# Performance work log

Measured on AMD Instinct MI355X. Metric: run time of the kernel, lower is better.

Reference implementation:

```python
import jax, jax.numpy as jnp
import numpy as np

EMBED_DIM = 1024
NUM_HEADS = 16
HEAD_DIM = EMBED_DIM // NUM_HEADS
BATCH = 2
SEQ = 2048


def setup_inputs() -> dict:
    key = jax.random.key(0)
    ks = jax.random.split(key, 10)
    s = 1.0 / np.sqrt(EMBED_DIM)
    inp = {
        "query": jax.random.normal(ks[0], (BATCH, SEQ, EMBED_DIM), jnp.float32),
        # Linear weights stored as [in, out] (y = x @ W + b)
        "wq": jax.random.normal(ks[1], (EMBED_DIM, EMBED_DIM), jnp.float32) * s,
        "bq": jnp.zeros((EMBED_DIM,), jnp.float32),
        "wk": jax.random.normal(ks[2], (EMBED_DIM, EMBED_DIM), jnp.float32) * s,
        "bk": jnp.zeros((EMBED_DIM,), jnp.float32),
        "wv": jax.random.normal(ks[3], (EMBED_DIM, EMBED_DIM), jnp.float32) * s,
        "bv": jnp.zeros((EMBED_DIM,), jnp.float32),
        "wo": jax.random.normal(ks[4], (EMBED_DIM, EMBED_DIM), jnp.float32) * s,
        "bo": jnp.zeros((EMBED_DIM,), jnp.float32),
        "temperature": jnp.float32(HEAD_DIM),  # learnable temperature, init = head_dim
    }
    return inp


def reference(query, wq, bq, wk, bk, wv, bv, wo, bo, temperature):
    B, S, E = query.shape
    # self-attention: key = value = query
    Q = (query @ wq + bq).reshape(B, S, NUM_HEADS, HEAD_DIM).transpose(0, 2, 1, 3)
    K = (query @ wk + bk).reshape(B, S, NUM_HEADS, HEAD_DIM).transpose(0, 2, 1, 3)
    V = (query @ wv + bv).reshape(B, S, NUM_HEADS, HEAD_DIM).transpose(0, 2, 1, 3)
    # squared Euclidean distances: ||q||^2 + ||k||^2 - 2<q,k>
    q_sq = jnp.sum(Q * Q, axis=-1, keepdims=True)          # (B,H,Sq,1)
    k_sq = jnp.sum(K * K, axis=-1, keepdims=True)          # (B,H,Sk,1)
    qk = jnp.einsum("bhqd,bhkd->bhqk", Q, K)
    d_sq = jnp.maximum(q_sq + jnp.swapaxes(k_sq, -2, -1) - 2.0 * qk, 0.0)
    attn = jax.nn.softmax(-d_sq / temperature, axis=-1)    # (B,H,Sq,Sk)
    out = jnp.einsum("bhqk,bhkd->bhqd", attn, V)
    out = out.transpose(0, 2, 1, 3).reshape(B, S, E)
    return out @ wo + bo
```

## Files before the change

kernel.cpp:

```cpp
#include <hip/hip_runtime.h>
#include <stdint.h>
#include <stddef.h>


#define LOG2E 1.44269504088896f

typedef __attribute__((ext_vector_type(8))) short bf16x8;
typedef __attribute__((ext_vector_type(4))) float f32x4;
typedef __attribute__((ext_vector_type(4))) unsigned short u16x4;

__device__ __forceinline__ unsigned short f2b(float f) {
  union { float f; unsigned int u; } x; x.f = f;
  unsigned int u = x.u;
  u += 0x7fffu + ((u >> 16) & 1u);
  return (unsigned short)(u >> 16);
}
__device__ __forceinline__ float b2f(unsigned short s) {
  union { unsigned int u; float f; } x; x.u = ((unsigned int)s) << 16;
  return x.f;
}
__device__ __forceinline__ unsigned int fbits(float f) {
  union { float f; unsigned int u; } x; x.f = f; return x.u;
}

#define GLD_LDS(g, l) __builtin_amdgcn_global_load_lds( \
    (const __attribute__((address_space(1))) void*)(g), \
    (__attribute__((address_space(3))) void*)(l), 16, 0, 0)

__global__ void prep_kernel(const float* __restrict__ X,
                            const float* __restrict__ wq, const float* __restrict__ wk,
                            const float* __restrict__ wv, const float* __restrict__ wo,
                            unsigned short* __restrict__ Xb,
                            unsigned short* __restrict__ WTqkv, unsigned short* __restrict__ WTo) {
  int z = blockIdx.z;
  if (z == 4) {
    size_t base = ((size_t)(blockIdx.y * 16 + blockIdx.x)) * 16384;
    #pragma unroll
    for (int j = 0; j < 16; ++j) {
      size_t i = base + (size_t)(j * 256 + threadIdx.x) * 4;
      f32x4 v = *(const f32x4*)&X[i];
      u16x4 o;
      #pragma unroll
      for (int k = 0; k < 4; ++k) o[k] = f2b(v[k]);
      *(u16x4*)&Xb[i] = o;
    }
    return;
  }
  __shared__ float tile[64][65];
  const float* src = (z == 0) ? wq : (z == 1) ? wk : (z == 2) ? wv : wo;
  unsigned short* dst = (z < 3) ? (WTqkv + (size_t)z * 1024 * 1024) : WTo;
  int k0 = blockIdx.y * 64, n0 = blockIdx.x * 64;
  int rr = threadIdx.x >> 6, cc = threadIdx.x & 63;
  #pragma unroll
  for (int p = 0; p < 16; ++p) {
    int row = p * 4 + rr;
    tile[row][cc] = src[(size_t)(k0 + row) * 1024 + n0 + cc];
  }
  __syncthreads();
  #pragma unroll
  for (int p = 0; p < 16; ++p) {
    int row = p * 4 + rr;
    dst[(size_t)(n0 + row) * 1024 + k0 + cc] = f2b(tile[cc][row]);
  }
}

__global__ __launch_bounds__(256, 3) void gemm_qkv_kernel(
    const unsigned short* __restrict__ X, const unsigned short* __restrict__ WT,
    const float* __restrict__ bq, const float* __restrict__ bk, const float* __restrict__ bv,
    const float* __restrict__ temp,
    unsigned short* __restrict__ Qb, unsigned short* __restrict__ Kb,
    unsigned short* __restrict__ VTo, float* __restrict__ ks2) {
  __shared__ __align__(16) unsigned short smem3[24576];
#define AS3(j) (smem3 + (j) * 4096)
#define BS3(j) (smem3 + 12288 + (j) * 4096)
  const int t = threadIdx.x, w = t >> 6, lane = t & 63;
  const int r = lane & 15, q4 = lane >> 4;
  const int m0 = blockIdx.y * 128, n0 = blockIdx.x * 128;
  const int wr = (w >> 1) * 64, wc = (w & 1) * 64;
  const unsigned short* Xg = X + (size_t)m0 * 1024;
  const unsigned short* Wg = WT + (size_t)n0 * 1024;
  const unsigned short* xs0 = Xg + (size_t)(t >> 2) * 1024 + (t & 3) * 8;
  const unsigned short* xs1 = xs0 + (size_t)64 * 1024;
  const unsigned short* ws0 = Wg + (size_t)(t >> 2) * 1024 + (t & 3) * 8;
  const unsigned short* ws1 = ws0 + (size_t)64 * 1024;
  f32x4 acc[4][4] = {};

#define QKV_STAGE(J2)                                     \
  {                                                       \
    GLD_LDS(xs0, &AS3(J2)[(w * 64) * 8]);                 \
    GLD_LDS(xs1, &AS3(J2)[(256 + w * 64) * 8]);           \
    GLD_LDS(ws0, &BS3(J2)[(w * 64) * 8]);                 \
    GLD_LDS(ws1, &BS3(J2)[(256 + w * 64) * 8]);           \
    xs0 += 32; xs1 += 32; ws0 += 32; ws1 += 32;           \
  }

  QKV_STAGE(0)
  QKV_STAGE(1)
  asm volatile("s_waitcnt vmcnt(4)" ::: "memory");
  __builtin_amdgcn_s_barrier();
  __builtin_amdgcn_sched_barrier(0);

#define QKV_BODY(J, STG, LAST)                                                \
  {                                                                           \
    if (STG) QKV_STAGE(((J) + 2) % 3)                                         \
    bf16x8 af[4], bfr[4];                                                     \
    _Pragma("unroll")                                                         \
    for (int mf = 0; mf < 4; ++mf)                                            \
      af[mf] = *(const bf16x8*)&AS3(J)[(wr + mf * 16 + r) * 32 + q4 * 8];     \
    _Pragma("unroll")                                                         \
    for (int nf = 0; nf < 4; ++nf)                                            \
      bfr[nf] = *(const bf16x8*)&BS3(J)[(wc + nf * 16 + r) * 32 + q4 * 8];    \
    _Pragma("unroll")                                                         \
    for (int mf = 0; mf < 4; ++mf)                                            \
      _Pragma("unroll")                                                       \
      for (int nf = 0; nf < 4; ++nf)                                          \
        acc[mf][nf] = __builtin_amdgcn_mfma_f32_16x16x32_bf16(af[mf], bfr[nf], acc[mf][nf], 0, 0, 0); \
    if (STG)       { asm volatile("s_waitcnt vmcnt(4)" ::: "memory"); }       \
    else if (!(LAST)) { asm volatile("s_waitcnt vmcnt(0)" ::: "memory"); }    \
    if (!(LAST)) {                                                            \
      __builtin_amdgcn_s_barrier();                                           \
      __builtin_amdgcn_sched_barrier(0);                                      \
    }                                                                         \
  }

  for (int hh = 0; hh < 5; ++hh) {
    QKV_BODY(0, 1, 0) QKV_BODY(1, 1, 0) QKV_BODY(2, 1, 0)
    QKV_BODY(0, 1, 0) QKV_BODY(1, 1, 0) QKV_BODY(2, 1, 0)
  }
  QKV_BODY(0, 0, 0)
  QKV_BODY(1, 0, 1)
  __syncthreads();
#undef QKV_BODY
#undef QKV_STAGE

  const int nblk = n0 >> 10;
  if (nblk == 0) {
    const int nc0 = n0 & 1023;
    #pragma unroll
    for (int nf = 0; nf < 4; ++nf) {
      int n = nc0 + wc + nf * 16 + r;
      float bb = bq[n];
      #pragma unroll
      for (int mf = 0; mf < 4; ++mf) {
        int m = m0 + wr + mf * 16 + q4 * 4;
        f32x4 v = acc[mf][nf];
        #pragma unroll
        for (int i = 0; i < 4; ++i)
          Qb[(size_t)(m + i) * 1024 + n] = f2b(v[i] + bb);
      }
    }
  } else if (nblk == 1) {
    const float sc = LOG2E / temp[0];
    const int nc0 = n0 & 1023;
    float s2a[4][4] = {};
    #pragma unroll
    for (int nf = 0; nf < 4; ++nf) {
      int n = nc0 + wc + nf * 16 + r;
      float bb = bk[n];
      #pragma unroll
      for (int mf = 0; mf < 4; ++mf) {
        int m = m0 + wr + mf * 16 + q4 * 4;
        f32x4 v = acc[mf][nf];
        #pragma unroll
        for (int i = 0; i < 4; ++i) {
          unsigned short os = f2b(v[i] + bb);
          Kb[(size_t)(m + i) * 1024 + n] = os;
          float xb = b2f(os);
          s2a[mf][i] += xb * xb;
        }
      }
    }
    #pragma unroll
    for (int mf = 0; mf < 4; ++mf)
      #pragma unroll
      for (int i = 0; i < 4; ++i) {
        float v = s2a[mf][i];
        v += __shfl_xor(v, 1, 64);
        v += __shfl_xor(v, 2, 64);
        v += __shfl_xor(v, 4, 64);
        v += __shfl_xor(v, 8, 64);
        s2a[mf][i] = v * sc;
      }
    if (r == 0) {
      int hh2 = (nc0 + wc) >> 6;
      #pragma unroll
      for (int mf = 0; mf < 4; ++mf) {
        int m = m0 + wr + mf * 16 + q4 * 4;
        int bb2 = m >> 11, ss = m & 2047;
        #pragma unroll
        for (int i = 0; i < 4; ++i)
          ks2[(size_t)(bb2 * 16 + hh2) * 2048 + ss + i] = s2a[mf][i];
      }
    }
  } else {
    unsigned short* Vt = smem3;
    const int c0 = n0 - 2048;
    const int head = w & 1;
    #pragma unroll
    for (int nf = 0; nf < 4; ++nf) {
      int c = c0 + wc + nf * 16 + r;
      float bb = bv[c];
      int d = c & 63;
      #pragma unroll
      for (int mf = 0; mf < 4; ++mf) {
        int mloc = wr + mf * 16 + q4 * 4;
        int G = mloc >> 6;
        int k6 = mloc & 63;
        int pos = (k6 >> 5) * 32 + ((k6 & 15) >> 2) * 8 + ((k6 >> 4) & 1) * 4;
        f32x4 v = acc[mf][nf];
        u16x4 pk;
        #pragma unroll
        for (int i = 0; i < 4; ++i) pk[i] = f2b(v[i] + bb);
        *(u16x4*)&Vt[(head * 64 + d) * 132 + G * 64 + pos] = pk;
      }
    }
    __syncthreads();
    int row = t >> 1, ch = t & 1;
    int hd = row >> 6, dd = row & 63;
    int hglob = (c0 >> 6) + hd;
    int bb2 = m0 >> 11, s0 = m0 & 2047;
    unsigned short* dst = &VTo[((size_t)((bb2 * 16 + hglob) * 64 + dd)) * 2048 + s0 + ch * 64];
    const unsigned short* srcL = &Vt[(hd * 64 + dd) * 132 + ch * 64];
    #pragma unroll
    for (int k2 = 0; k2 < 16; ++k2)
      *(u16x4*)&dst[k2 * 4] = *(const u16x4*)&srcL[k2 * 4];
  }
#undef AS3
#undef BS3
}

__global__ __launch_bounds__(256, 2) void flash_kernel(
    const unsigned short* __restrict__ Qb, const unsigned short* __restrict__ Kb,
    const unsigned short* __restrict__ VT, const float* __restrict__ ks2,
    const float* __restrict__ temp, unsigned short* __restrict__ AO) {
  __shared__ __align__(16) unsigned short Ks[2][64 * 64];
  __shared__ __align__(16) unsigned short Vs[3][64 * 64];
  __shared__ __align__(16) float KQs[2048];
  const int t = threadIdx.x, w = t >> 6, lane = t & 63;
  const int r = lane & 15, q4 = lane >> 4;
  const int wgid = blockIdx.x + 16 * blockIdx.y;
  const int xcd = wgid & 7, s = wgid >> 3;
  const int bh = xcd + 8 * (s & 3);
  const int b = bh >> 4, h = bh & 15;
  const int q0 = (s >> 2) * 128;
  const float cc = 2.0f * LOG2E / temp[0];

  bf16x8 qf[2][2];
  #pragma unroll
  for (int qg = 0; qg < 2; ++qg) {
    int sq = q0 + w * 32 + qg * 16 + r;
    const unsigned short* qp = Qb + (size_t)(b * 2048 + sq) * 1024 + h * 64;
    #pragma unroll
    for (int ks = 0; ks < 2; ++ks) qf[qg][ks] = *(const bf16x8*)(qp + ks * 32 + q4 * 8);
  }

  f32x4 accO[2][4] = {};
  f32x4 lsum[2] = {};
  bf16x8 ones;
  #pragma unroll
  for (int j = 0; j < 8; ++j) ones[j] = (short)0x3F80;

  const unsigned short* Kg = Kb + ((size_t)b * 2048) * 1024 + h * 64;
  const unsigned short* Vg = VT + ((size_t)bh * 64) * 2048;
  const float* kqb = ks2 + bh * 2048;

  const unsigned short* kp0 = Kg + (size_t)(t >> 2) * 1024 + (t & 3) * 8;
  const unsigned short* kp1 = kp0 + 32;
  int dd0 = t >> 3;
  const unsigned short* vp0 = Vg + (size_t)dd0 * 2048 + ((t & 7) ^ (dd0 & 7)) * 8;
  const unsigned short* vp1 = vp0 + (size_t)32 * 2048;

  GLD_LDS(kqb + t * 4, &KQs[t * 4]);
  GLD_LDS(kqb + 1024 + t * 4, &KQs[1024 + t * 4]);
  GLD_LDS(kp0, &Ks[0][t * 8]);
  GLD_LDS(kp1, &Ks[0][(256 + t) * 8]);
  GLD_LDS(vp0, &Vs[0][t * 8]);
  GLD_LDS(vp1, &Vs[0][(256 + t) * 8]);
  kp0 += 65536; kp1 += 65536; vp0 += 64; vp1 += 64;
  GLD_LDS(kp0, &Ks[1][t * 8]);
  GLD_LDS(kp1, &Ks[1][(256 + t) * 8]);
  GLD_LDS(vp0, &Vs[1][t * 8]);
  GLD_LDS(vp1, &Vs[1][(256 + t) * 8]);
  kp0 += 65536; kp1 += 65536; vp0 += 64; vp1 += 64;

  const unsigned short* v_cur = &Vs[0][0];
  const unsigned short* v_nxt = &Vs[1][0];
  const unsigned short* v_fre = &Vs[2][0];

  asm volatile("s_waitcnt vmcnt(4)" ::: "memory");
  __builtin_amdgcn_s_barrier();
  __builtin_amdgcn_sched_barrier(0);

  f32x4 stA[2][4], stB[2][4];
  {
    const f32x4 zz = {};
    __builtin_amdgcn_s_setprio(1);
    #pragma unroll
    for (int ks = 0; ks < 2; ++ks) {
      #pragma unroll
      for (int kfm = 0; kfm < 4; ++kfm) {
        bf16x8 ka = *(const bf16x8*)&Ks[0][(ks * 64 + kfm * 16 + r) * 32 + q4 * 8];
        stA[0][kfm] = __builtin_amdgcn_mfma_f32_16x16x32_bf16(ka, qf[0][ks], ks ? stA[0][kfm] : zz, 0, 0, 0);
        stA[1][kfm] = __builtin_amdgcn_mfma_f32_16x16x32_bf16(ka, qf[1][ks], ks ? stA[1][kfm] : zz, 0, 0, 0);
      }
    }
    __builtin_amdgcn_s_setprio(0);
  }

#define CHUNK_BODY(C, STC, STN)                                               \
  {                                                                           \
    const int c_ = (C);                                                       \
    __builtin_amdgcn_s_barrier();                                             \
    if (c_ < 30) {                                                            \
      unsigned short* kdst = &Ks[(C) & 1][0];                                 \
      GLD_LDS(kp0, kdst + t * 8);                                             \
      GLD_LDS(kp1, kdst + (256 + t) * 8);                                     \
      GLD_LDS(vp0, (unsigned short*)v_fre + t * 8);                           \
      GLD_LDS(vp1, (unsigned short*)v_fre + (256 + t) * 8);                   \
      kp0 += 65536; kp1 += 65536; vp0 += 64; vp1 += 64;                       \
      asm volatile("s_waitcnt vmcnt(4)" ::: "memory");                        \
    } else {                                                                  \
      asm volatile("s_waitcnt vmcnt(0)" ::: "memory");                        \
    }                                                                         \
    __builtin_amdgcn_s_barrier();                                             \
    __builtin_amdgcn_sched_barrier(0);                                        \
                 \
    if (c_ < 31) {                                                            \
      const unsigned short* krd = &Ks[((C) + 1) & 1][0];                      \
      const f32x4 zz = {};                                                    \
      __builtin_amdgcn_s_setprio(1);                                          \
      _Pragma("unroll")                                                       \
      for (int ks = 0; ks < 2; ++ks) {                                        \
        _Pragma("unroll")                                                     \
        for (int kfm = 0; kfm < 4; ++kfm) {                                   \
          bf16x8 ka = *(const bf16x8*)&krd[(ks * 64 + kfm * 16 + r) * 32 + q4 * 8]; \
          STN[0][kfm] = __builtin_amdgcn_mfma_f32_16x16x32_bf16(ka, qf[0][ks], ks ? STN[0][kfm] : zz, 0, 0, 0); \
          STN[1][kfm] = __builtin_amdgcn_mfma_f32_16x16x32_bf16(ka, qf[1][ks], ks ? STN[1][kfm] : zz, 0, 0, 0); \
        }                                                                     \
      }                                                                       \
      __builtin_amdgcn_s_setprio(0);                                          \
    }                                                                         \
                                \
    f32x4 kq[4];                                                              \
    _Pragma("unroll")                                                         \
    for (int kfm = 0; kfm < 4; ++kfm)                                         \
      kq[kfm] = *(const f32x4*)&KQs[c_ * 64 + kfm * 16 + q4 * 4];             \
    bf16x8 pf[2][2];                                                          \
    _Pragma("unroll")                                                         \
    for (int qg = 0; qg < 2; ++qg) {                                          \
      _Pragma("unroll")                                                       \
      for (int cb = 0; cb < 2; ++cb) {                                        \
        unsigned int dw[4];                                                   \
        _Pragma("unroll")                                                     \
        for (int half = 0; half < 2; ++half) {                                \
          int kfm = cb * 2 + half;                                            \
          float pp[4];                                                        \
          _Pragma("unroll")                                                   \
          for (int i = 0; i < 4; ++i) {                                       \
            float u = __builtin_fmaf(cc, STC[qg][kfm][i], -kq[kfm][i]);       \
            pp[i] = __builtin_amdgcn_exp2f(u);                                \
          }                                                                   \
          dw[half * 2 + 0] = (fbits(pp[0]) >> 16) | (fbits(pp[1]) & 0xFFFF0000u); \
          dw[half * 2 + 1] = (fbits(pp[2]) >> 16) | (fbits(pp[3]) & 0xFFFF0000u); \
        }                                                                     \
        union { unsigned int d[4]; bf16x8 v; } cv;                            \
        cv.d[0] = dw[0]; cv.d[1] = dw[1]; cv.d[2] = dw[2]; cv.d[3] = dw[3];   \
        pf[qg][cb] = cv.v;                                                    \
      }                                                                       \
    }                                                                         \
        \
    __builtin_amdgcn_s_setprio(1);                                            \
    _Pragma("unroll")                                                         \
    for (int cb = 0; cb < 2; ++cb) {                                          \
      lsum[0] = __builtin_amdgcn_mfma_f32_16x16x32_bf16(pf[0][cb], ones, lsum[0], 0, 0, 0); \
      lsum[1] = __builtin_amdgcn_mfma_f32_16x16x32_bf16(pf[1][cb], ones, lsum[1], 0, 0, 0); \
      _Pragma("unroll")                                                       \
      for (int df = 0; df < 4; ++df) {                                        \
        int dloc = df * 16 + r;                                               \
        int un = dloc * 8 + ((cb * 4 + q4) ^ (dloc & 7));                     \
        bf16x8 vb = *(const bf16x8*)&v_cur[un * 8];                           \
        accO[0][df] = __builtin_amdgcn_mfma_f32_16x16x32_bf16(pf[0][cb], vb, accO[0][df], 0, 0, 0); \
        accO[1][df] = __builtin_amdgcn_mfma_f32_16x16x32_bf16(pf[1][cb], vb, accO[1][df], 0, 0, 0); \
      }                                                                       \
    }                                                                         \
    __builtin_amdgcn_s_setprio(0);                                            \
    const unsigned short* tv = v_cur; v_cur = v_nxt; v_nxt = v_fre; v_fre = tv; \
  }

  for (int c2 = 0; c2 < 16; ++c2) {
    CHUNK_BODY(2 * c2, stA, stB)
    CHUNK_BODY(2 * c2 + 1, stB, stA)
  }
#undef CHUNK_BODY

  {
    #pragma unroll
    for (int qg = 0; qg < 2; ++qg) {
      float inv[4];
      #pragma unroll
      for (int i = 0; i < 4; ++i) inv[i] = 1.0f / lsum[qg][i];
      #pragma unroll
      for (int df = 0; df < 4; ++df) {
        int d = df * 16 + r;
        #pragma unroll
        for (int i = 0; i < 4; ++i) {
          int sq = q0 + w * 32 + qg * 16 + q4 * 4 + i;
          AO[(size_t)(b * 2048 + sq) * 1024 + h * 64 + d] = f2b(accO[qg][df][i] * inv[i]);
        }
      }
    }
  }
}

__global__ __launch_bounds__(256, 2) void gemm_out_kernel(
    const unsigned short* __restrict__ A, const unsigned short* __restrict__ WT,
    const float* __restrict__ bo, float* __restrict__ Out) {
  __shared__ __align__(16) unsigned short osmem[18432];
#define AS3o(j) (osmem + (j) * 4096)
#define BS3o(j) (osmem + 12288 + (j) * 2048)
  const int t = threadIdx.x, w = t >> 6, lane = t & 63;
  const int r = lane & 15, q4 = lane >> 4;
  const int m0 = blockIdx.y * 128, n0 = blockIdx.x * 64;
  const int wr = (w >> 1) * 64, wc = (w & 1) * 32;
  const unsigned short* Ag = A + (size_t)m0 * 1024;
  const unsigned short* Wg = WT + (size_t)n0 * 1024;
  const unsigned short* as0 = Ag + (size_t)(t >> 2) * 1024 + (t & 3) * 8;
  const unsigned short* as1 = as0 + (size_t)64 * 1024;
  const unsigned short* bs0 = Wg + (size_t)(t >> 2) * 1024 + (t & 3) * 8;
  f32x4 acc[4][2] = {};

#define OUT_STAGE(J2)                                     \
  {                                                       \
    GLD_LDS(as0, &AS3o(J2)[(w * 64) * 8]);                \
    GLD_LDS(as1, &AS3o(J2)[(256 + w * 64) * 8]);          \
    GLD_LDS(bs0, &BS3o(J2)[(w * 64) * 8]);                \
    as0 += 32; as1 += 32; bs0 += 32;                      \
  }

  OUT_STAGE(0)
  OUT_STAGE(1)
  asm volatile("s_waitcnt vmcnt(3)" ::: "memory");
  __builtin_amdgcn_s_barrier();
  __builtin_amdgcn_sched_barrier(0);

#define OUT_BODY(J, STG, LAST)                                                \
  {                                                                           \
    if (STG) OUT_STAGE(((J) + 2) % 3)                                         \
    bf16x8 af[4], bfr[2];                                                     \
    _Pragma("unroll")                                                         \
    for (int mf = 0; mf < 4; ++mf)                                            \
      af[mf] = *(const bf16x8*)&AS3o(J)[(wr + mf * 16 + r) * 32 + q4 * 8];    \
    _Pragma("unroll")                                                         \
    for (int nf = 0; nf < 2; ++nf)                                            \
      bfr[nf] = *(const bf16x8*)&BS3o(J)[(wc + nf * 16 + r) * 32 + q4 * 8];   \
    _Pragma("unroll")                                                         \
    for (int mf = 0; mf < 4; ++mf)                                            \
      _Pragma("unroll")                                                       \
      for (int nf = 0; nf < 2; ++nf)                                          \
        acc[mf][nf] = __builtin_amdgcn_mfma_f32_16x16x32_bf16(af[mf], bfr[nf], acc[mf][nf], 0, 0, 0); \
    if (STG)       { asm volatile("s_waitcnt vmcnt(3)" ::: "memory"); }       \
    else if (!(LAST)) { asm volatile("s_waitcnt vmcnt(0)" ::: "memory"); }    \
    if (!(LAST)) {                                                            \
      __builtin_amdgcn_s_barrier();                                           \
      __builtin_amdgcn_sched_barrier(0);                                      \
    }                                                                         \
  }

  for (int hh = 0; hh < 5; ++hh) {
    OUT_BODY(0, 1, 0) OUT_BODY(1, 1, 0) OUT_BODY(2, 1, 0)
    OUT_BODY(0, 1, 0) OUT_BODY(1, 1, 0) OUT_BODY(2, 1, 0)
  }
  OUT_BODY(0, 0, 0)
  OUT_BODY(1, 0, 1)
#undef OUT_BODY
#undef OUT_STAGE
#undef AS3o
#undef BS3o

  #pragma unroll
  for (int nf = 0; nf < 2; ++nf) {
    int n = n0 + wc + nf * 16 + r;
    float bb = bo[n];
    #pragma unroll
    for (int mf = 0; mf < 4; ++mf) {
      int m = m0 + wr + mf * 16 + q4 * 4;
      f32x4 v = acc[mf][nf];
      #pragma unroll
      for (int i = 0; i < 4; ++i)
        Out[(size_t)(m + i) * 1024 + n] = v[i] + bb;
    }
  }
}

extern "C" void kernel_launch(void* const* d_in, const int* in_sizes, int n_in,
                              void* d_out, int out_size, void* d_ws, size_t ws_size,
                              hipStream_t stream) {
  const float* X    = (const float*)d_in[0];
  const float* wq   = (const float*)d_in[1];
  const float* bq   = (const float*)d_in[2];
  const float* wk   = (const float*)d_in[3];
  const float* bk   = (const float*)d_in[4];
  const float* wv   = (const float*)d_in[5];
  const float* bv   = (const float*)d_in[6];
  const float* wo   = (const float*)d_in[7];
  const float* bo   = (const float*)d_in[8];
  const float* temp = (const float*)d_in[9];
  float* Out = (float*)d_out;

  char* ws = (char*)d_ws;
  unsigned short* Xb    = (unsigned short*)ws; ws += (size_t)4096 * 1024 * 2;
  unsigned short* WTqkv = (unsigned short*)ws; ws += (size_t)3072 * 1024 * 2;
  unsigned short* WTo   = (unsigned short*)ws; ws += (size_t)1024 * 1024 * 2;
  unsigned short* Qb    = (unsigned short*)ws; ws += (size_t)4096 * 1024 * 2;
  unsigned short* Kb    = (unsigned short*)ws; ws += (size_t)4096 * 1024 * 2;
  unsigned short* VT    = (unsigned short*)ws; ws += (size_t)4096 * 1024 * 2;
  float* ks2 = (float*)ws; ws += (size_t)65536 * 4;
  unsigned short* AO = Xb;

  prep_kernel<<<dim3(16, 16, 5), 256, 0, stream>>>(X, wq, wk, wv, wo, Xb, WTqkv, WTo);
  gemm_qkv_kernel<<<dim3(24, 32), 256, 0, stream>>>(Xb, WTqkv, bq, bk, bv, temp, Qb, Kb, VT, ks2);
  flash_kernel<<<dim3(16, 32), 256, 0, stream>>>(Qb, Kb, VT, ks2, temp, AO);
  gemm_out_kernel<<<dim3(16, 32), 256, 0, stream>>>(AO, WTo, bo, Out);
}
```

Before: 184.9 us.

## Triple-buffer K tiles and use one barrier per chunk in flash loop

K tiles move from double to triple buffering in LDS, matching V, and the loop is unrolled by three with static buffer indices instead of rotating pointers. The software-pipelined QK^T for the next chunk is removed: each chunk computes its own scores, then waits and hits a single barrier at the end instead of two per chunk. This cuts barrier count and register pressure from two score sets, but loses the overlap of next-chunk QK MFMAs with the softmax and uses more LDS, which may affect occupancy at two blocks per CU.

```diff
diff --git a/kernel.cpp b/kernel.cpp
--- a/kernel.cpp
+++ b/kernel.cpp
@@ -233,7 +233,7 @@
     const unsigned short* __restrict__ Qb, const unsigned short* __restrict__ Kb,
     const unsigned short* __restrict__ VT, const float* __restrict__ ks2,
     const float* __restrict__ temp, unsigned short* __restrict__ AO) {
-  __shared__ __align__(16) unsigned short Ks[2][64 * 64];
+  __shared__ __align__(16) unsigned short Ks[3][64 * 64];
   __shared__ __align__(16) unsigned short Vs[3][64 * 64];
   __shared__ __align__(16) float KQs[2048];
   const int t = threadIdx.x, w = t >> 6, lane = t & 63;
@@ -282,65 +282,37 @@
   GLD_LDS(vp0, &Vs[1][t * 8]);
   GLD_LDS(vp1, &Vs[1][(256 + t) * 8]);
   kp0 += 65536; kp1 += 65536; vp0 += 64; vp1 += 64;
-
-  const unsigned short* v_cur = &Vs[0][0];
-  const unsigned short* v_nxt = &Vs[1][0];
-  const unsigned short* v_fre = &Vs[2][0];
-
   asm volatile("s_waitcnt vmcnt(4)" ::: "memory");
   __builtin_amdgcn_s_barrier();
   __builtin_amdgcn_sched_barrier(0);
 
-  f32x4 stA[2][4], stB[2][4];
-  {
-    const f32x4 zz = {};
-    __builtin_amdgcn_s_setprio(1);
-    #pragma unroll
-    for (int ks = 0; ks < 2; ++ks) {
-      #pragma unroll
-      for (int kfm = 0; kfm < 4; ++kfm) {
-        bf16x8 ka = *(const bf16x8*)&Ks[0][(ks * 64 + kfm * 16 + r) * 32 + q4 * 8];
-        stA[0][kfm] = __builtin_amdgcn_mfma_f32_16x16x32_bf16(ka, qf[0][ks], ks ? stA[0][kfm] : zz, 0, 0, 0);
-        stA[1][kfm] = __builtin_amdgcn_mfma_f32_16x16x32_bf16(ka, qf[1][ks], ks ? stA[1][kfm] : zz, 0, 0, 0);
-      }
-    }
-    __builtin_amdgcn_s_setprio(0);
-  }
-
-#define CHUNK_BODY(C, STC, STN)                                               \
+#define CHUNK_BODY(C, J, STG, LAST)                                           \
   {                                                                           \
     const int c_ = (C);                                                       \
-    __builtin_amdgcn_s_barrier();                                             \
-    if (c_ < 30) {                                                            \
-      unsigned short* kdst = &Ks[(C) & 1][0];                                 \
-      GLD_LDS(kp0, kdst + t * 8);                                             \
-      GLD_LDS(kp1, kdst + (256 + t) * 8);                                     \
-      GLD_LDS(vp0, (unsigned short*)v_fre + t * 8);                           \
-      GLD_LDS(vp1, (unsigned short*)v_fre + (256 + t) * 8);                   \
+    if (STG) {                                                                \
+      GLD_LDS(kp0, &Ks[((J) + 2) % 3][t * 8]);                                \
+      GLD_LDS(kp1, &Ks[((J) + 2) % 3][(256 + t) * 8]);                        \
+      GLD_LDS(vp0, &Vs[((J) + 2) % 3][t * 8]);                                \
+      GLD_LDS(vp1, &Vs[((J) + 2) % 3][(256 + t) * 8]);                        \
       kp0 += 65536; kp1 += 65536; vp0 += 64; vp1 += 64;                       \
-      asm volatile("s_waitcnt vmcnt(4)" ::: "memory");                        \
-    } else {                                                                  \
-      asm volatile("s_waitcnt vmcnt(0)" ::: "memory");                        \
-    }                                                                         \
-    __builtin_amdgcn_s_barrier();                                             \
-    __builtin_amdgcn_sched_barrier(0);                                        \
-                 \
-    if (c_ < 31) {                                                            \
-      const unsigned short* krd = &Ks[((C) + 1) & 1][0];                      \
+    }                                                                         \
+          \
+    f32x4 st[2][4];                                                           \
+    {                                                                         \
       const f32x4 zz = {};                                                    \
       __builtin_amdgcn_s_setprio(1);                                          \
       _Pragma("unroll")                                                       \
       for (int ks = 0; ks < 2; ++ks) {                                        \
         _Pragma("unroll")                                                     \
         for (int kfm = 0; kfm < 4; ++kfm) {                                   \
-          bf16x8 ka = *(const bf16x8*)&krd[(ks * 64 + kfm * 16 + r) * 32 + q4 * 8]; \
-          STN[0][kfm] = __builtin_amdgcn_mfma_f32_16x16x32_bf16(ka, qf[0][ks], ks ? STN[0][kfm] : zz, 0, 0, 0); \
-          STN[1][kfm] = __builtin_amdgcn_mfma_f32_16x16x32_bf16(ka, qf[1][ks], ks ? STN[1][kfm] : zz, 0, 0, 0); \
+          bf16x8 ka = *(const bf16x8*)&Ks[(J)][(ks * 64 + kfm * 16 + r) * 32 + q4 * 8]; \
+          st[0][kfm] = __builtin_amdgcn_mfma_f32_16x16x32_bf16(ka, qf[0][ks], ks ? st[0][kfm] : zz, 0, 0, 0); \
+          st[1][kfm] = __builtin_amdgcn_mfma_f32_16x16x32_bf16(ka, qf[1][ks], ks ? st[1][kfm] : zz, 0, 0, 0); \
         }                                                                     \
       }                                                                       \
       __builtin_amdgcn_s_setprio(0);                                          \
     }                                                                         \
-                                \
+                 \
     f32x4 kq[4];                                                              \
     _Pragma("unroll")                                                         \
     for (int kfm = 0; kfm < 4; ++kfm)                                         \
@@ -357,7 +329,7 @@
           float pp[4];                                                        \
           _Pragma("unroll")                                                   \
           for (int i = 0; i < 4; ++i) {                                       \
-            float u = __builtin_fmaf(cc, STC[qg][kfm][i], -kq[kfm][i]);       \
+            float u = __builtin_fmaf(cc, st[qg][kfm][i], -kq[kfm][i]);        \
             pp[i] = __builtin_amdgcn_exp2f(u);                                \
           }                                                                   \
           dw[half * 2 + 0] = (fbits(pp[0]) >> 16) | (fbits(pp[1]) & 0xFFFF0000u); \
@@ -368,7 +340,7 @@
         pf[qg][cb] = cv.v;                                                    \
       }                                                                       \
     }                                                                         \
-        \
+                                        \
     __builtin_amdgcn_s_setprio(1);                                            \
     _Pragma("unroll")                                                         \
     for (int cb = 0; cb < 2; ++cb) {                                          \
@@ -378,19 +350,28 @@
       for (int df = 0; df < 4; ++df) {                                        \
         int dloc = df * 16 + r;                                               \
         int un = dloc * 8 + ((cb * 4 + q4) ^ (dloc & 7));                     \
-        bf16x8 vb = *(const bf16x8*)&v_cur[un * 8];                           \
+        bf16x8 vb = *(const bf16x8*)&Vs[(J)][un * 8];                         \
         accO[0][df] = __builtin_amdgcn_mfma_f32_16x16x32_bf16(pf[0][cb], vb, accO[0][df], 0, 0, 0); \
         accO[1][df] = __builtin_amdgcn_mfma_f32_16x16x32_bf16(pf[1][cb], vb, accO[1][df], 0, 0, 0); \
       }                                                                       \
     }                                                                         \
     __builtin_amdgcn_s_setprio(0);                                            \
-    const unsigned short* tv = v_cur; v_cur = v_nxt; v_nxt = v_fre; v_fre = tv; \
-  }
-
-  for (int c2 = 0; c2 < 16; ++c2) {
-    CHUNK_BODY(2 * c2, stA, stB)
-    CHUNK_BODY(2 * c2 + 1, stB, stA)
-  }
+                             \
+    if (STG)          { asm volatile("s_waitcnt vmcnt(4)" ::: "memory"); }    \
+    else if (!(LAST)) { asm volatile("s_waitcnt vmcnt(0)" ::: "memory"); }    \
+    if (!(LAST)) {                                                            \
+      __builtin_amdgcn_s_barrier();                                           \
+      __builtin_amdgcn_sched_barrier(0);                                      \
+    }                                                                         \
+  }
+
+  for (int c3 = 0; c3 < 10; ++c3) {
+    CHUNK_BODY(3 * c3 + 0, 0, 1, 0)
+    CHUNK_BODY(3 * c3 + 1, 1, 1, 0)
+    CHUNK_BODY(3 * c3 + 2, 2, 1, 0)
+  }
+  CHUNK_BODY(30, 0, 0, 0)
+  CHUNK_BODY(31, 1, 0, 1)
 #undef CHUNK_BODY
 
   {
```

Result: no change. 186.8 us (+1.0%).
